# Optimization experiments

Measured on AMD Instinct MI355X. Metric: run time of the kernel, lower is better.

The kernel has to match this reference:

```python
import jax, jax.numpy as jnp
import numpy as np


def setup_inputs() -> dict:
    key = jax.random.key(0)
    k_u, k_dt, k_A, k_B, k_C = jax.random.split(key, 5)
    batch, seq_len, d_model = 8, 4096, 1024
    u = jax.random.normal(k_u, (batch, seq_len, d_model), dtype=jnp.float32)
    # delta is a positive discretization step size
    delta = jax.random.uniform(k_dt, (batch, seq_len, d_model), dtype=jnp.float32,
                               minval=0.001, maxval=0.1)
    # A initialized in [-1.0, -0.1] so exp(A*delta) in (0,1) (stable decay)
    A = jax.random.uniform(k_A, (d_model,), dtype=jnp.float32, minval=-1.0, maxval=-0.1)
    B = jax.random.normal(k_B, (batch, seq_len, d_model), dtype=jnp.float32)
    C = jax.random.normal(k_C, (batch, seq_len, d_model), dtype=jnp.float32)
    return {"u": u, "delta": delta, "A": A, "B": B, "C": C}


def _selective_scan(u, delta, A, B, C):
    # Per-channel SSM with scalar state (N=1):
    #   a_t = exp(A * delta_t)           (decay factor, in (0,1))
    #   h_t = a_t * h_{t-1} + delta_t * B_t * u_t
    #   y_t = C_t * h_t
    a = jnp.exp(delta * A)          # [b, s, d]
    b = delta * B * u               # [b, s, d]

    def combine(left, right):
        a1, b1 = left
        a2, b2 = right
        return a1 * a2, a2 * b1 + b2

    _, h = jax.lax.associative_scan(combine, (a, b), axis=1)  # [b, s, d]
    return C * h


def reference(u, delta, A, B, C):
    return _selective_scan(u, delta, A, B, C)
```

## Files before the change

### kernel.cpp

```cpp
#include <hip/hip_runtime.h>


#define BB 8
#define SS 4096
#define DD 1024
#define TT 16
#define NCHUNK (SS / TT)
#define NBLK   (BB * NCHUNK)

__global__ __launch_bounds__(256) void k1_local(
    const float* __restrict__ u, const float* __restrict__ delta,
    const float* __restrict__ A, const float* __restrict__ Bm,
    float* __restrict__ aggA, float* __restrict__ aggB)
{
    const int c = blockIdx.x % NCHUNK;
    const int b = blockIdx.x / NCHUNK;
    const int d4 = threadIdx.x << 2;

    const float4 Av = *(const float4*)(A + d4);
    size_t idx = ((size_t)(b * SS + c * TT)) * DD + d4;

    float4 h = {0.f, 0.f, 0.f, 0.f};
    float4 p = {1.f, 1.f, 1.f, 1.f};
#pragma unroll 4
    for (int t = 0; t < TT; ++t, idx += DD) {
        const float4 dt = *(const float4*)(delta + idx);
        const float4 bv = *(const float4*)(Bm + idx);
        const float4 uv = *(const float4*)(u + idx);
        float a;
        a = __expf(dt.x * Av.x); h.x = fmaf(a, h.x, dt.x * bv.x * uv.x); p.x *= a;
        a = __expf(dt.y * Av.y); h.y = fmaf(a, h.y, dt.y * bv.y * uv.y); p.y *= a;
        a = __expf(dt.z * Av.z); h.z = fmaf(a, h.z, dt.z * bv.z * uv.z); p.z *= a;
        a = __expf(dt.w * Av.w); h.w = fmaf(a, h.w, dt.w * bv.w * uv.w); p.w *= a;
    }
    const size_t o = ((size_t)(b * NCHUNK + c)) * DD + d4;
    *(float4*)(aggA + o) = p;
    *(float4*)(aggB + o) = h;
}

__global__ __launch_bounds__(256) void k2_scan(
    const float* __restrict__ aggA, float* __restrict__ aggB)
{
    const int chain = blockIdx.x * 4 + (threadIdx.x >> 6);
    const int lane  = threadIdx.x & 63;
    const int b = chain >> 10;
    const int d = chain & 1023;
    const size_t base = (size_t)b * NCHUNK * DD + (size_t)d;
    const int c0 = lane << 2;

    float a0, a1, a2, a3, b0, b1, b2, b3;
    {
        size_t o = base + (size_t)c0 * DD;
        a0 = aggA[o]; b0 = aggB[o]; o += DD;
        a1 = aggA[o]; b1 = aggB[o]; o += DD;
        a2 = aggA[o]; b2 = aggB[o]; o += DD;
        a3 = aggA[o]; b3 = aggB[o];
    }
    const float A01 = a0 * a1, B01 = fmaf(a1, b0, b1);
    const float A23 = a2 * a3, B23 = fmaf(a3, b2, b3);
    float Aa = A01 * A23;
    float Bb = fmaf(A23, B01, B23);
#pragma unroll
    for (int s = 1; s < 64; s <<= 1) {
        const float Ap = __shfl_up(Aa, s);
        const float Bp = __shfl_up(Bb, s);
        if (lane >= s) { Bb = fmaf(Aa, Bp, Bb); Aa *= Ap; }
    }
    float X0 = __shfl_up(Bb, 1);
    if (lane == 0) X0 = 0.0f;
    const float X1 = fmaf(a0, X0, b0);
    const float X2 = fmaf(a1, X1, b1);
    const float X3 = fmaf(a2, X2, b2);
    size_t o = base + (size_t)c0 * DD;
    aggB[o] = X0; o += DD;
    aggB[o] = X1; o += DD;
    aggB[o] = X2; o += DD;
    aggB[o] = X3;
}

__global__ __launch_bounds__(256) void k3_apply(
    const float* __restrict__ u, const float* __restrict__ delta,
    const float* __restrict__ A, const float* __restrict__ Bm,
    const float* __restrict__ Cm, const float* __restrict__ pref,
    float* __restrict__ out)
{
    const int c = blockIdx.x % NCHUNK;
    const int b = blockIdx.x / NCHUNK;
    const int d4 = threadIdx.x << 2;

    const float4 Av = *(const float4*)(A + d4);
    float4 h = *(const float4*)(pref + ((size_t)(b * NCHUNK + c)) * DD + d4);

    size_t idx = ((size_t)(b * SS + c * TT)) * DD + d4;
#pragma unroll 4
    for (int t = 0; t < TT; ++t, idx += DD) {
        const float4 dt = *(const float4*)(delta + idx);
        const float4 bv = *(const float4*)(Bm + idx);
        const float4 uv = *(const float4*)(u + idx);
        const float4 cv = *(const float4*)(Cm + idx);
        float a; float4 y;
        a = __expf(dt.x * Av.x); h.x = fmaf(a, h.x, dt.x * bv.x * uv.x); y.x = cv.x * h.x;
        a = __expf(dt.y * Av.y); h.y = fmaf(a, h.y, dt.y * bv.y * uv.y); y.y = cv.y * h.y;
        a = __expf(dt.z * Av.z); h.z = fmaf(a, h.z, dt.z * bv.z * uv.z); y.z = cv.z * h.z;
        a = __expf(dt.w * Av.w); h.w = fmaf(a, h.w, dt.w * bv.w * uv.w); y.w = cv.w * h.w;
        *(float4*)(out + idx) = y;
    }
}

extern "C" void kernel_launch(void* const* d_in, const int* in_sizes, int n_in,
                              void* d_out, int out_size, void* d_ws, size_t ws_size,
                              hipStream_t stream) {
    (void)in_sizes; (void)n_in; (void)out_size; (void)ws_size;
    const float* u     = (const float*)d_in[0];
    const float* delta = (const float*)d_in[1];
    const float* A     = (const float*)d_in[2];
    const float* Bm    = (const float*)d_in[3];
    const float* Cm    = (const float*)d_in[4];
    float* out = (float*)d_out;

    float* ws = (float*)d_ws;
    const size_t n = (size_t)BB * NCHUNK * DD;
    float* aggA = ws;
    float* aggB = ws + n;

    k1_local<<<NBLK, 256, 0, stream>>>(u, delta, A, Bm, aggA, aggB);
    k2_scan<<<BB * DD / 4, 256, 0, stream>>>(aggA, aggB);
    k3_apply<<<NBLK, 256, 0, stream>>>(u, delta, A, Bm, Cm, aggB, out);
}
```

Measured before the change: 268.0 us.

## Software-pipeline chunk loads, serialize chunk-prefix scan per channel, nontemporal output stores

The local and apply kernels now fully unroll the 16-step chunk loop and prefetch inputs two steps ahead through a rotating register buffer, so memory latency overlaps the exp/fma chain. The middle kernel swaps the per-chain wavefront shuffle scan for a plain sequential loop over 256 chunks per (batch, channel). Each thread owns one channel, so loads coalesce across the 64-lane block, and results go to a separate prefix buffer. Output stores use nontemporal hints to avoid polluting cache. The serial scan has a long dependency chain and launches only 128 small blocks, which may leave the GPU underused in that phase.

Measured after the change: 244.8 us. -8.7%, faster.

```diff
diff --git a/kernel.cpp b/kernel.cpp
--- a/kernel.cpp
+++ b/kernel.cpp
@@ -8,6 +8,22 @@
 #define NCHUNK (SS / TT)
 #define NBLK   (BB * NCHUNK)
 
+typedef __attribute__((ext_vector_type(4))) float f32x4;
+
+__device__ __forceinline__ float4 ld4(const float* __restrict__ p) {
+    return *(const float4*)p;
+}
+
+__device__ __forceinline__ void scan_step(float4& h, float4& p,
+                                          const float4 dt, const float4 bv,
+                                          const float4 uv, const float4 Av) {
+    float a;
+    a = __expf(dt.x * Av.x); h.x = fmaf(a, h.x, dt.x * bv.x * uv.x); p.x *= a;
+    a = __expf(dt.y * Av.y); h.y = fmaf(a, h.y, dt.y * bv.y * uv.y); p.y *= a;
+    a = __expf(dt.z * Av.z); h.z = fmaf(a, h.z, dt.z * bv.z * uv.z); p.z *= a;
+    a = __expf(dt.w * Av.w); h.w = fmaf(a, h.w, dt.w * bv.w * uv.w); p.w *= a;
+}
+
 __global__ __launch_bounds__(256) void k1_local(
     const float* __restrict__ u, const float* __restrict__ delta,
     const float* __restrict__ A, const float* __restrict__ Bm,
@@ -17,65 +33,47 @@
     const int b = blockIdx.x / NCHUNK;
     const int d4 = threadIdx.x << 2;
 
-    const float4 Av = *(const float4*)(A + d4);
-    size_t idx = ((size_t)(b * SS + c * TT)) * DD + d4;
+    const float4 Av = ld4(A + d4);
+    const size_t base = ((size_t)(b * SS + c * TT)) * DD + d4;
 
     float4 h = {0.f, 0.f, 0.f, 0.f};
     float4 p = {1.f, 1.f, 1.f, 1.f};
-#pragma unroll 4
-    for (int t = 0; t < TT; ++t, idx += DD) {
-        const float4 dt = *(const float4*)(delta + idx);
-        const float4 bv = *(const float4*)(Bm + idx);
-        const float4 uv = *(const float4*)(u + idx);
-        float a;
-        a = __expf(dt.x * Av.x); h.x = fmaf(a, h.x, dt.x * bv.x * uv.x); p.x *= a;
-        a = __expf(dt.y * Av.y); h.y = fmaf(a, h.y, dt.y * bv.y * uv.y); p.y *= a;
-        a = __expf(dt.z * Av.z); h.z = fmaf(a, h.z, dt.z * bv.z * uv.z); p.z *= a;
-        a = __expf(dt.w * Av.w); h.w = fmaf(a, h.w, dt.w * bv.w * uv.w); p.w *= a;
+
+    float4 dt[3], bv[3], uv[3];
+    dt[0] = ld4(delta + base);      bv[0] = ld4(Bm + base);      uv[0] = ld4(u + base);
+    dt[1] = ld4(delta + base + DD); bv[1] = ld4(Bm + base + DD); uv[1] = ld4(u + base + DD);
+#pragma unroll
+    for (int t = 0; t < TT; ++t) {
+        if (t + 2 < TT) {
+            const int s2 = (t + 2) % 3;
+            const size_t i2 = base + (size_t)(t + 2) * DD;
+            dt[s2] = ld4(delta + i2);
+            bv[s2] = ld4(Bm + i2);
+            uv[s2] = ld4(u + i2);
+        }
+        const int s = t % 3;
+        scan_step(h, p, dt[s], bv[s], uv[s], Av);
     }
     const size_t o = ((size_t)(b * NCHUNK + c)) * DD + d4;
     *(float4*)(aggA + o) = p;
     *(float4*)(aggB + o) = h;
 }
 
-__global__ __launch_bounds__(256) void k2_scan(
-    const float* __restrict__ aggA, float* __restrict__ aggB)
+__global__ __launch_bounds__(64) void k2_scan(
+    const float* __restrict__ aggA, const float* __restrict__ aggB,
+    float* __restrict__ pref)
 {
-    const int chain = blockIdx.x * 4 + (threadIdx.x >> 6);
-    const int lane  = threadIdx.x & 63;
-    const int b = chain >> 10;
-    const int d = chain & 1023;
+    const int b = blockIdx.x >> 4;
+    const int d = ((blockIdx.x & 15) << 6) + threadIdx.x;
     const size_t base = (size_t)b * NCHUNK * DD + (size_t)d;
-    const int c0 = lane << 2;
 
-    float a0, a1, a2, a3, b0, b1, b2, b3;
-    {
-        size_t o = base + (size_t)c0 * DD;
-        a0 = aggA[o]; b0 = aggB[o]; o += DD;
-        a1 = aggA[o]; b1 = aggB[o]; o += DD;
-        a2 = aggA[o]; b2 = aggB[o]; o += DD;
-        a3 = aggA[o]; b3 = aggB[o];
+    float X = 0.f;
+#pragma unroll 8
+    for (int c = 0; c < NCHUNK; ++c) {
+        const size_t o = base + (size_t)c * DD;
+        pref[o] = X;
+        X = fmaf(aggA[o], X, aggB[o]);
     }
-    const float A01 = a0 * a1, B01 = fmaf(a1, b0, b1);
-    const float A23 = a2 * a3, B23 = fmaf(a3, b2, b3);
-    float Aa = A01 * A23;
-    float Bb = fmaf(A23, B01, B23);
-#pragma unroll
-    for (int s = 1; s < 64; s <<= 1) {
-        const float Ap = __shfl_up(Aa, s);
-        const float Bp = __shfl_up(Bb, s);
-        if (lane >= s) { Bb = fmaf(Aa, Bp, Bb); Aa *= Ap; }
-    }
-    float X0 = __shfl_up(Bb, 1);
-    if (lane == 0) X0 = 0.0f;
-    const float X1 = fmaf(a0, X0, b0);
-    const float X2 = fmaf(a1, X1, b1);
-    const float X3 = fmaf(a2, X2, b2);
-    size_t o = base + (size_t)c0 * DD;
-    aggB[o] = X0; o += DD;
-    aggB[o] = X1; o += DD;
-    aggB[o] = X2; o += DD;
-    aggB[o] = X3;
 }
 
 __global__ __launch_bounds__(256) void k3_apply(
@@ -88,22 +86,31 @@
     const int b = blockIdx.x / NCHUNK;
     const int d4 = threadIdx.x << 2;
 
-    const float4 Av = *(const float4*)(A + d4);
-    float4 h = *(const float4*)(pref + ((size_t)(b * NCHUNK + c)) * DD + d4);
+    const float4 Av = ld4(A + d4);
+    float4 h = ld4(pref + ((size_t)(b * NCHUNK + c)) * DD + d4);
+    const size_t base = ((size_t)(b * SS + c * TT)) * DD + d4;
 
-    size_t idx = ((size_t)(b * SS + c * TT)) * DD + d4;
-#pragma unroll 4
-    for (int t = 0; t < TT; ++t, idx += DD) {
-        const float4 dt = *(const float4*)(delta + idx);
-        const float4 bv = *(const float4*)(Bm + idx);
-        const float4 uv = *(const float4*)(u + idx);
-        const float4 cv = *(const float4*)(Cm + idx);
-        float a; float4 y;
-        a = __expf(dt.x * Av.x); h.x = fmaf(a, h.x, dt.x * bv.x * uv.x); y.x = cv.x * h.x;
-        a = __expf(dt.y * Av.y); h.y = fmaf(a, h.y, dt.y * bv.y * uv.y); y.y = cv.y * h.y;
-        a = __expf(dt.z * Av.z); h.z = fmaf(a, h.z, dt.z * bv.z * uv.z); y.z = cv.z * h.z;
-        a = __expf(dt.w * Av.w); h.w = fmaf(a, h.w, dt.w * bv.w * uv.w); y.w = cv.w * h.w;
-        *(float4*)(out + idx) = y;
+    float4 dt[3], bv[3], uv[3], cv[2];
+    float4 dump = {0.f, 0.f, 0.f, 0.f};
+    dt[0] = ld4(delta + base);      bv[0] = ld4(Bm + base);      uv[0] = ld4(u + base);
+    dt[1] = ld4(delta + base + DD); bv[1] = ld4(Bm + base + DD); uv[1] = ld4(u + base + DD);
+    cv[0] = ld4(Cm + base);
+#pragma unroll
+    for (int t = 0; t < TT; ++t) {
+        if (t + 2 < TT) {
+            const int s2 = (t + 2) % 3;
+            const size_t i2 = base + (size_t)(t + 2) * DD;
+            dt[s2] = ld4(delta + i2);
+            bv[s2] = ld4(Bm + i2);
+            uv[s2] = ld4(u + i2);
+        }
+        if (t + 1 < TT) cv[(t + 1) % 2] = ld4(Cm + base + (size_t)(t + 1) * DD);
+        const int s = t % 3;
+        scan_step(h, dump, dt[s], bv[s], uv[s], Av);
+        const float4 c4 = cv[t % 2];
+        f32x4 y;
+        y.x = c4.x * h.x; y.y = c4.y * h.y; y.z = c4.z * h.z; y.w = c4.w * h.w;
+        __builtin_nontemporal_store(y, (f32x4*)(out + base + (size_t)t * DD));
     }
 }
 
@@ -122,8 +129,9 @@
     const size_t n = (size_t)BB * NCHUNK * DD;
     float* aggA = ws;
     float* aggB = ws + n;
+    float* pref = ws + 2 * n;
 
     k1_local<<<NBLK, 256, 0, stream>>>(u, delta, A, Bm, aggA, aggB);
-    k2_scan<<<BB * DD / 4, 256, 0, stream>>>(aggA, aggB);
-    k3_apply<<<NBLK, 256, 0, stream>>>(u, delta, A, Bm, Cm, aggB, out);
+    k2_scan<<<BB * (DD / 64), 64, 0, stream>>>(aggA, aggB, pref);
+    k3_apply<<<NBLK, 256, 0, stream>>>(u, delta, A, Bm, Cm, pref, out);
 }
```
